# Performance work log

Measured on AMD Instinct MI355X. Metric: run time of the kernel, lower is better.

Reference implementation:

```python
import jax, jax.numpy as jnp
import numpy as np

# ---- config (mirrors init_kwargs) ----
H = 128
W = 128
FMO_STEPS = 4
INPUT_FRAMES = 1
N_PIECES = 1
N_TERMS = 2
CAM_DIST = 2.0
ROT_DIVIDE = 1.0
SIGMAINV = 7000.0
ERODE_K = 5
FOCAL = float(1.0 / np.tan(1.57 / 4.0))  # generate_perspective_projection(1.57/2), aspect=1


def quaternion_to_angle_axis(q):
    # q: [B,4] in (w,x,y,z) convention (torchgeometry)
    q1, q2, q3 = q[..., 1], q[..., 2], q[..., 3]
    sin_sq = q1 * q1 + q2 * q2 + q3 * q3
    sin_t = jnp.sqrt(sin_sq + 1e-20)
    cos_t = q[..., 0]
    two_theta = 2.0 * jnp.where(cos_t < 0.0, jnp.arctan2(-sin_t, -cos_t), jnp.arctan2(sin_t, cos_t))
    k = jnp.where(sin_sq > 1e-12, two_theta / sin_t, 2.0)
    return q[..., 1:4] * k[..., None]


def angle_axis_to_rotation_matrix(aa):
    # aa: [B,3] -> [B,3,3] (Rodrigues)
    th = jnp.sqrt(jnp.sum(aa * aa, axis=-1, keepdims=True) + 1e-12)  # [B,1]
    k = aa / th
    kx, ky, kz = k[..., 0], k[..., 1], k[..., 2]
    zero = jnp.zeros_like(kx)
    K = jnp.stack([jnp.stack([zero, -kz, ky], -1),
                   jnp.stack([kz, zero, -kx], -1),
                   jnp.stack([-ky, kx, zero], -1)], -2)
    s = jnp.sin(th)[..., None]
    c = jnp.cos(th)[..., None]
    return jnp.eye(3, dtype=aa.dtype) + s * K + (1.0 - c) * jnp.matmul(K, K)


def rasterize(fv_img, fv_z, face_feat, fn_z):
    # fv_img [B,F,3,2] NDC, fv_z [B,F,3] camera z, face_feat [B,F,3,C], fn_z [B,F]
    B, F = fv_img.shape[:2]
    xs = jnp.linspace(-1.0, 1.0, W)
    ys = jnp.linspace(1.0, -1.0, H)
    py, px = jnp.meshgrid(ys, xs, indexing='ij')  # [H,W]
    a, b, c = fv_img[:, :, 0], fv_img[:, :, 1], fv_img[:, :, 2]  # [B,F,2]
    e0 = b - a
    e1 = c - a
    denom = e0[..., 0] * e1[..., 1] - e0[..., 1] * e1[..., 0]  # [B,F]
    valid = (fn_z > 0.0) & (jnp.abs(denom) > 1e-10)
    inv_den = jnp.where(jnp.abs(denom) > 1e-10, 1.0 / denom, 0.0)
    dx = px[None, None] - a[..., 0][..., None, None]  # [B,F,H,W]
    dy = py[None, None] - a[..., 1][..., None, None]
    w1 = (dx * e1[..., 1][..., None, None] - dy * e1[..., 0][..., None, None]) * inv_den[..., None, None]
    w2 = (e0[..., 0][..., None, None] * dy - e0[..., 1][..., None, None] * dx) * inv_den[..., None, None]
    w0 = 1.0 - w1 - w2
    inside = (w0 >= 0.0) & (w1 >= 0.0) & (w2 >= 0.0) & valid[..., None, None]
    zi = (w0 * fv_z[:, :, 0, None, None] + w1 * fv_z[:, :, 1, None, None] + w2 * fv_z[:, :, 2, None, None])
    score = jnp.where(inside, zi, -1e10)  # camera looks down -z: nearest face has max z
    best = jnp.argmax(score, axis=1)      # [B,H,W] z-buffer winner
    hit = jnp.any(inside, axis=1)
    bary = jnp.stack([w0, w1, w2], axis=-1)  # [B,F,H,W,3]
    idx = jnp.broadcast_to(best[:, None, :, :, None], (B, 1, H, W, 3))
    bary_b = jnp.take_along_axis(bary, idx, axis=1)[:, 0]  # [B,H,W,3]
    feat_b = jax.vmap(lambda f, i: f[i])(face_feat, best)  # [B,H,W,3,C]
    feats = jnp.einsum('bhwkc,bhwk->bhwc', feat_b, bary_b) * hit[..., None]
    # DIB-R soft silhouette: A = 1 - prod(1 - exp(-sigmainv*d^2)), d = dist to triangle, 0 inside
    d2 = None
    tri = (a, b, c)
    for i in range(3):
        p, q = tri[i], tri[(i + 1) % 3]
        ex = (q - p)[..., 0][..., None, None]
        ey = (q - p)[..., 1][..., None, None]
        rx = px[None, None] - p[..., 0][..., None, None]
        ry = py[None, None] - p[..., 1][..., None, None]
        L2 = ex * ex + ey * ey + 1e-12
        t = jnp.clip((rx * ex + ry * ey) / L2, 0.0, 1.0)
        dxe = rx - t * ex
        dye = ry - t * ey
        dd = dxe * dxe + dye * dye
        d2 = dd if d2 is None else jnp.minimum(d2, dd)
    d2 = jnp.where(inside, 0.0, d2)
    prob = jnp.where(valid[..., None, None], jnp.exp(-SIGMAINV * d2), 0.0)
    mask = 1.0 - jnp.prod(1.0 - prob, axis=1)  # [B,H,W]
    return feats, mask


def texture_sample(tex, uv):
    # tex [B,3,Th,Tw], uv [B,H,W,2] in [0,1]; bilinear, v axis flipped (image row 0 <-> v=1)
    Th, Tw = tex.shape[2], tex.shape[3]
    u = jnp.clip(uv[..., 0], 0.0, 1.0) * (Tw - 1)
    v = (1.0 - jnp.clip(uv[..., 1], 0.0, 1.0)) * (Th - 1)
    x0 = jnp.floor(u)
    y0 = jnp.floor(v)
    fx = (u - x0)[:, None]  # [B,1,H,W]
    fy = (v - y0)[:, None]
    x0i = jnp.clip(x0.astype(jnp.int32), 0, Tw - 1)
    x1i = jnp.clip(x0i + 1, 0, Tw - 1)
    y0i = jnp.clip(y0.astype(jnp.int32), 0, Th - 1)
    y1i = jnp.clip(y0i + 1, 0, Th - 1)
    g = jax.vmap(lambda t, yy, xx: t[:, yy, xx])  # [B,3,H,W]
    t00 = g(tex, y0i, x0i)
    t01 = g(tex, y0i, x1i)
    t10 = g(tex, y1i, x0i)
    t11 = g(tex, y1i, x1i)
    return t00 * (1 - fx) * (1 - fy) + t01 * fx * (1 - fy) + t10 * (1 - fx) * fy + t11 * fx * fy


def erode(m, k):
    # kornia erosion with an all-ones kxk kernel == min-pool (geodesic border)
    return -jax.lax.reduce_window(-m, -jnp.inf, jax.lax.max, (1, k, k), (1, 1, 1), 'SAME')


def render_frame(verts_world, faces, face_features, texture_maps):
    # camera at (0,0,CAM_DIST) looking at origin with up=(0,1,0): R_cam == I
    v_cam = verts_world - jnp.array([0.0, 0.0, CAM_DIST], dtype=verts_world.dtype)
    fv_cam = v_cam[:, faces]  # [B,F,3,3]
    n = jnp.cross(fv_cam[:, :, 1] - fv_cam[:, :, 0], fv_cam[:, :, 2] - fv_cam[:, :, 0])
    n = n / (jnp.linalg.norm(n, axis=-1, keepdims=True) + 1e-10)
    fn_z = n[..., 2]
    z = fv_cam[..., 2]  # negative in front of camera
    img = FOCAL * fv_cam[..., :2] / (-z[..., None] + 1e-10)  # [B,F,3,2]
    uv, mask = rasterize(img, z, face_features, fn_z)
    rgb = texture_sample(texture_maps, uv)  # [B,3,H,W]
    mask_e = erode(mask, ERODE_K)
    return jnp.concatenate([rgb, mask_e[:, None]], axis=1)  # [B,4,H,W]


def reference(vertices, translation, quaternion, exp, face_features, texture_maps, faces):
    rot = angle_axis_to_rotation_matrix(quaternion_to_angle_axis(quaternion[:, 0, 0]))
    trans_start = translation[:, :, 0, 0]  # [B,1,3]
    all_renders = []
    renders = []
    frames = 0
    time_before = 0.0
    for pind in range(N_PIECES):
        angles = quaternion_to_angle_axis(quaternion[:, pind, 1]) / ROT_DIVIDE
        rot_step = angle_axis_to_rotation_matrix(exp * angles / FMO_STEPS)
        rot_noexp = angle_axis_to_rotation_matrix(angles * (1.0 - exp))
        n_steps = FMO_STEPS * INPUT_FRAMES // N_PIECES  # prop[pind] (forced for single piece)
        for ti in np.linspace(0.0, 1.0, n_steps):
            if frames == 0:
                time_before = ti
            time_exp = time_before + (ti - time_before) * exp  # [1]
            verts = jnp.einsum('bij,bvj->bvi', rot, vertices) + trans_start
            for p in range(1, N_TERMS):
                verts = verts + (time_exp ** p) * translation[:, :, pind, p]
            renders.append(render_frame(verts, faces, face_features, texture_maps))
            frames += 1
            if frames == FMO_STEPS:
                frames = 0
                all_renders.append(jnp.stack(renders, 1))
                renders = []
                rot = jnp.matmul(rot, rot_noexp)
            else:
                rot = jnp.matmul(rot, rot_step)
        for p in range(1, N_TERMS):
            trans_start = trans_start + translation[:, :, pind, p]
    return jnp.stack(all_renders, 1)  # [B, input_frames, fmo_steps, 4, H, W]


def setup_inputs() -> dict:
    key = jax.random.key(0)
    ks = jax.random.split(key, 7)
    B, V, F = 1, 162, 320
    vertices = jax.random.normal(ks[0], (B, V, 3), jnp.float32) * 0.3
    translation = jax.random.normal(ks[1], (B, 1, N_PIECES, N_TERMS, 3), jnp.float32) * 0.1
    quaternion = jax.random.normal(ks[2], (B, N_PIECES, 2, 4), jnp.float32)
    exp = jax.random.uniform(ks[3], (1,), jnp.float32)
    face_features = jax.random.uniform(ks[4], (B, F, 3, 2), jnp.float32)
    texture_maps = jax.random.uniform(ks[5], (B, 3, 256, 256), jnp.float32)
    faces = jax.random.randint(ks[6], (F, 3), 0, V)
    return {"vertices": vertices, "translation": translation, "quaternion": quaternion,
            "exp": exp, "face_features": face_features, "texture_maps": texture_maps,
            "faces": faces}
```

## Files before the change

### kernel.cpp

```cpp
#include <hip/hip_runtime.h>
#include <math.h>

#define N_FRAMES 4
#define N_FACES  320
#define N_VERTS  162
#define IMG_H    128
#define IMG_W    128
#define FD_STRIDE 24
#define NWAVES   8



__device__ __forceinline__ void q_to_aa(const float* q, float* aa) {
    float q1 = q[1], q2 = q[2], q3 = q[3];
    float sin_sq = (q1 * q1 + q2 * q2) + q3 * q3;
    float sin_t = sqrtf(sin_sq + 1e-20f);
    float cos_t = q[0];
    float two_theta = (cos_t < 0.0f) ? (2.0f * atan2f(-sin_t, -cos_t))
                                     : (2.0f * atan2f(sin_t, cos_t));
    float k = (sin_sq > 1e-12f) ? (two_theta / sin_t) : 2.0f;
    aa[0] = q1 * k; aa[1] = q2 * k; aa[2] = q3 * k;
}

__device__ __forceinline__ void aa_to_R(const float* aa, float* R) {
    float th = sqrtf(((aa[0] * aa[0] + aa[1] * aa[1]) + aa[2] * aa[2]) + 1e-12f);
    float kx = aa[0] / th, ky = aa[1] / th, kz = aa[2] / th;
    float K[9] = { 0.0f, -kz,  ky,
                   kz,  0.0f, -kx,
                  -ky,   kx, 0.0f };
    float s = sinf(th), c = cosf(th);
    float KK[9];
    for (int i = 0; i < 3; ++i)
        for (int j = 0; j < 3; ++j)
            KK[i*3+j] = (K[i*3+0] * K[0*3+j] + K[i*3+1] * K[1*3+j]) + K[i*3+2] * K[2*3+j];
    float omc = 1.0f - c;
    for (int i = 0; i < 9; ++i) {
        float eye = (i == 0 || i == 4 || i == 8) ? 1.0f : 0.0f;
        R[i] = (eye + s * K[i]) + omc * KK[i];
    }
}

__device__ __forceinline__ void mat3mul(const float* A, const float* B, float* C) {
    for (int i = 0; i < 3; ++i)
        for (int j = 0; j < 3; ++j)
            C[i*3+j] = (A[i*3+0] * B[0*3+j] + A[i*3+1] * B[1*3+j]) + A[i*3+2] * B[2*3+j];
}


__global__ void __launch_bounds__(256)
setup_kernel(const float* __restrict__ verts_in,
             const float* __restrict__ transl,
             const float* __restrict__ quat,
             const float* __restrict__ expv,
             const int*   __restrict__ faces,
             int*   __restrict__ faceCount,
             float* __restrict__ faceData)
{
    __shared__ float rots[N_FRAMES][9];
    __shared__ float sv[N_FRAMES][N_VERTS * 3];
    int tid = threadIdx.x;

    if (tid == 0) {
        float aa0[3], aa1[3], R0[9], step[9];
        q_to_aa(quat, aa0);
        aa_to_R(aa0, R0);
        q_to_aa(quat + 4, aa1);
        float e = expv[0];
        float arg[3];
        for (int i = 0; i < 3; ++i) arg[i] = (e * aa1[i]) / 4.0f;
        aa_to_R(arg, step);
        float cur[9];
        for (int i = 0; i < 9; ++i) { cur[i] = R0[i]; rots[0][i] = R0[i]; }
        for (int k = 1; k < N_FRAMES; ++k) {
            float nxt[9];
            mat3mul(cur, step, nxt);
            for (int i = 0; i < 9; ++i) { cur[i] = nxt[i]; rots[k][i] = nxt[i]; }
        }
    }
    __syncthreads();

    float e = expv[0];
    float t0 = transl[0], t1 = transl[1], t2 = transl[2];
    float u0 = transl[3], u1 = transl[4], u2 = transl[5];

    for (int item = tid; item < N_FRAMES * N_VERTS; item += blockDim.x) {
        int k = item / N_VERTS, v = item - k * N_VERTS;
        float te = (float)((double)k / 3.0) * e;
        float vx = verts_in[v*3+0], vy = verts_in[v*3+1], vz = verts_in[v*3+2];
        const float* R = rots[k];
        float dx_ = (R[0] * vx + R[1] * vy) + R[2] * vz;
        float dy_ = (R[3] * vx + R[4] * vy) + R[5] * vz;
        float dz_ = (R[6] * vx + R[7] * vy) + R[8] * vz;
        float x = (dx_ + t0) + te * u0;
        float y = (dy_ + t1) + te * u1;
        float z = (dz_ + t2) + te * u2;
        z = z - 2.0f;
        sv[k][v*3+0] = x; sv[k][v*3+1] = y; sv[k][v*3+2] = z;
    }
    __syncthreads();

    const float FOCAL = (float)(1.0 / tan(1.57 / 4.0));

    int w    = tid >> 6;
    int lane = tid & 63;
    unsigned long long lmask = (lane == 63) ? 0x7fffffffffffffffull
                                            : ((1ull << lane) - 1ull);
    int cnt = 0;
    for (int base = 0; base < N_FACES; base += 64) {
        int f = base + lane;
        int i0 = faces[f*3+0], i1 = faces[f*3+1], i2 = faces[f*3+2];
        const float* A = &sv[w][i0*3];
        const float* B = &sv[w][i1*3];
        const float* C = &sv[w][i2*3];
        float ux = B[0] - A[0], uy = B[1] - A[1];
        float wx = C[0] - A[0], wy = C[1] - A[1];
        float nz = ux * wy - uy * wx;
        float da = -A[2] + 1e-10f, db = -B[2] + 1e-10f, dc = -C[2] + 1e-10f;
        float ax = (FOCAL * A[0]) / da, ay = (FOCAL * A[1]) / da;
        float bx = (FOCAL * B[0]) / db, by = (FOCAL * B[1]) / db;
        float cx = (FOCAL * C[0]) / dc, cy = (FOCAL * C[1]) / dc;
        float e0x = bx - ax, e0y = by - ay;
        float e1x = cx - ax, e1y = cy - ay;
        float e12x = cx - bx, e12y = cy - by;
        float den = e0x * e1y - e0y * e1x;
        bool dok = fabsf(den) > 1e-10f;
        bool valid = dok && (nz > 0.0f);
        unsigned long long m = __ballot(valid);
        if (valid) {
            float invden = 1.0f / den;
            float L2_0 = (e0x * e0x + e0y * e0y) + 1e-12f;
            float L2_1 = (e12x * e12x + e12y * e12y) + 1e-12f;
            float L2_2 = (e1x * e1x + e1y * e1y) + 1e-12f;
            int pos = cnt + __popcll(m & lmask);
            float4* fd = (float4*)(faceData + (w * N_FACES + pos) * FD_STRIDE);
            fd[0] = make_float4(ax, ay, e0x, e0y);
            fd[1] = make_float4(e1x, e1y, invden, (float)f);
            fd[2] = make_float4(A[2], B[2], C[2], 1.0f / L2_0);
            fd[3] = make_float4(bx, by, e12x, e12y);
            fd[4] = make_float4(cx, cy, 1.0f / L2_1, 1.0f / L2_2);
            fd[5] = make_float4(fminf(fminf(ax, bx), cx), fminf(fminf(ay, by), cy),
                                fmaxf(fmaxf(ax, bx), cx), fmaxf(fmaxf(ay, by), cy));
        }
        cnt += __popcll(m);
    }
    if (lane == 0) faceCount[w] = cnt;
}


__global__ void __launch_bounds__(512)
raster_kernel(const int*   __restrict__ faceCount,
              const float* __restrict__ faceData,
              const float* __restrict__ ffeat,
              const float* __restrict__ tex,
              float* __restrict__ out,
              float* __restrict__ maskbuf)
{
    int frame = blockIdx.x >> 8;
    int blk   = blockIdx.x & 255;
    int tid   = threadIdx.x;
    int lane  = tid & 63;
    int wv    = __builtin_amdgcn_readfirstlane(tid >> 6);
    int tile_x = blk & 7, tile_y = blk >> 3;
    int j = tile_x * 16 + (lane & 15);
    int i = tile_y * 4 + (lane >> 4);

    int nv = faceCount[frame];

    float px = (float)(-1.0 + 2.0 * (double)j / 127.0);
    float py = (float)( 1.0 - 2.0 * (double)i / 127.0);

    float best = -1e10f;
    int bestf = 0;
    float bw0 = 0.0f, bw1 = 0.0f, bw2 = 0.0f;
    float P = 1.0f;

    const float* g = faceData + frame * N_FACES * FD_STRIDE;

    for (int f = wv; f < nv; f += NWAVES) {
        const float* d = g + f * FD_STRIDE;
        float xmin = d[20], ymin = d[21], xmax = d[22], ymax = d[23];
        float cdx = fmaxf(fmaxf(xmin - px, px - xmax), 0.0f);
        float cdy = fmaxf(fmaxf(ymin - py, py - ymax), 0.0f);
        bool near = (cdx * cdx + cdy * cdy) <= 0.003f;
        if (!__any(near)) continue;

        float ax = d[0], ay = d[1], e0x = d[2], e0y = d[3];
        float e1x = d[4], e1y = d[5], invden = d[6], fidx = d[7];
        float z0 = d[8], z1 = d[9], z2 = d[10], invL2_0 = d[11];
        float bx = d[12], by = d[13], e12x = d[14], e12y = d[15];
        float cx = d[16], cy = d[17], invL2_1 = d[18], invL2_2 = d[19];

        float dx = px - ax, dy = py - ay;
        float w1 = (dx * e1y - dy * e1x) * invden;
        float w2 = (e0x * dy - e0y * dx) * invden;
        float w0 = (1.0f - w1) - w2;
        bool inside = (w0 >= 0.0f) & (w1 >= 0.0f) & (w2 >= 0.0f);
        float zi = (w0 * z0 + w1 * z1) + w2 * z2;
        float score = inside ? zi : -1e10f;
        if (score > best) {
            best = score; bestf = (int)fidx; bw0 = w0; bw1 = w1; bw2 = w2;
        }

        float t0 = fminf(fmaxf((dx * e0x + dy * e0y) * invL2_0, 0.0f), 1.0f);
        float x0 = dx - t0 * e0x, y0 = dy - t0 * e0y;
        float dd = x0 * x0 + y0 * y0;
        float rx1 = px - bx, ry1 = py - by;
        float t1 = fminf(fmaxf((rx1 * e12x + ry1 * e12y) * invL2_1, 0.0f), 1.0f);
        float x1 = rx1 - t1 * e12x, y1 = ry1 - t1 * e12y;
        dd = fminf(dd, x1 * x1 + y1 * y1);
        float ex2 = -e1x, ey2 = -e1y;
        float rx2 = px - cx, ry2 = py - cy;
        float t2 = fminf(fmaxf((rx2 * ex2 + ry2 * ey2) * invL2_2, 0.0f), 1.0f);
        float x2 = rx2 - t2 * ex2, y2 = ry2 - t2 * ey2;
        dd = fminf(dd, x2 * x2 + y2 * y2);

        float d2 = inside ? 0.0f : dd;
        float prob = __expf(-7000.0f * d2);
        P *= (1.0f - prob);
    }

    __shared__ float red[512 * 6];
    float* my = &red[tid * 6];
    my[0] = best; my[1] = __int_as_float(bestf);
    my[2] = bw0;  my[3] = bw1; my[4] = bw2; my[5] = P;
    __syncthreads();

    if (tid < 64) {
        float bb = red[tid * 6 + 0];
        int   bf = __float_as_int(red[tid * 6 + 1]);
        float r0 = red[tid * 6 + 2], r1 = red[tid * 6 + 3], r2 = red[tid * 6 + 4];
        float Pt = red[tid * 6 + 5];
        for (int w = 1; w < NWAVES; ++w) {
            const float* e = &red[(w * 64 + tid) * 6];
            float s = e[0]; int ff = __float_as_int(e[1]);
            if ((s > bb) || ((s == bb) && (ff < bf))) {
                bb = s; bf = ff; r0 = e[2]; r1 = e[3]; r2 = e[4];
            }
            Pt *= e[5];
        }

        bool hit = bb != -1e10f;
        float uv0 = 0.0f, uv1 = 0.0f;
        if (hit) {
            const float* fp = ffeat + bf * 6;
            uv0 = (fp[0] * r0 + fp[2] * r1) + fp[4] * r2;
            uv1 = (fp[1] * r0 + fp[3] * r1) + fp[5] * r2;
        }
        float u = fminf(fmaxf(uv0, 0.0f), 1.0f) * 255.0f;
        float v = (1.0f - fminf(fmaxf(uv1, 0.0f), 1.0f)) * 255.0f;
        float x0f = floorf(u), y0f = floorf(v);
        float fx = u - x0f, fy = v - y0f;
        int x0i = min(max((int)x0f, 0), 255);
        int x1i = min(x0i + 1, 255);
        int y0i = min(max((int)y0f, 0), 255);
        int y1i = min(y0i + 1, 255);

        for (int c = 0; c < 3; ++c) {
            const float* tc = tex + c * 65536;
            float t00 = tc[y0i * 256 + x0i];
            float t01 = tc[y0i * 256 + x1i];
            float t10 = tc[y1i * 256 + x0i];
            float t11 = tc[y1i * 256 + x1i];
            float val = (t00 * (1.0f - fx)) * (1.0f - fy);
            val = val + (t01 * fx) * (1.0f - fy);
            val = val + (t10 * (1.0f - fx)) * fy;
            val = val + (t11 * fx) * fy;
            out[((frame * 4 + c) * IMG_H + i) * IMG_W + j] = val;
        }
        maskbuf[(frame * IMG_H + i) * IMG_W + j] = 1.0f - Pt;
    }
}


__global__ void __launch_bounds__(256)
erode_kernel(const float* __restrict__ maskbuf, float* __restrict__ out)
{
    int frame = blockIdx.x >> 6;
    int pix = (blockIdx.x & 63) * 256 + threadIdx.x;
    int i = pix >> 7, j = pix & 127;
    float m = 1e30f;
    for (int di = -2; di <= 2; ++di) {
        int ii = i + di;
        if (ii < 0 || ii >= IMG_H) continue;
        for (int dj = -2; dj <= 2; ++dj) {
            int jj = j + dj;
            if (jj < 0 || jj >= IMG_W) continue;
            m = fminf(m, maskbuf[(frame * IMG_H + ii) * IMG_W + jj]);
        }
    }
    out[((frame * 4 + 3) * IMG_H + i) * IMG_W + j] = m;
}


extern "C" void kernel_launch(void* const* d_in, const int* in_sizes, int n_in,
                              void* d_out, int out_size, void* d_ws, size_t ws_size,
                              hipStream_t stream) {
    const float* vertices      = (const float*)d_in[0];
    const float* translation   = (const float*)d_in[1];
    const float* quaternion    = (const float*)d_in[2];
    const float* expv          = (const float*)d_in[3];
    const float* face_features = (const float*)d_in[4];
    const float* texture_maps  = (const float*)d_in[5];
    const int*   faces         = (const int*)d_in[6];
    float* out = (float*)d_out;

    int*   faceCount = (int*)d_ws;
    float* faceData  = (float*)d_ws + 4;
    float* maskbuf   = faceData + N_FRAMES * N_FACES * FD_STRIDE;

    setup_kernel<<<1, 256, 0, stream>>>(vertices, translation, quaternion, expv,
                                        faces, faceCount, faceData);
    raster_kernel<<<N_FRAMES * 256, 512, 0, stream>>>(faceCount, faceData,
                                                      face_features, texture_maps,
                                                      out, maskbuf);
    erode_kernel<<<N_FRAMES * 64, 256, 0, stream>>>(maskbuf, out);
}
```

Measured before the change: 91.67 us.

## Fuse face setup into raster kernel with per-block LDS face records and tile culling

```diff
diff --git a/kernel.cpp b/kernel.cpp
--- a/kernel.cpp
+++ b/kernel.cpp
@@ -6,8 +6,15 @@
 #define N_VERTS  162
 #define IMG_H    128
 #define IMG_W    128
-#define FD_STRIDE 24
 #define NWAVES   8
+#define FPW      40
+#define REC_SZ   20
+
+#define SV_OFF   0
+#define BB_OFF   1952
+#define BB_LD    48
+#define REC_OFF  8096
+#define ARENA_SZ 33696
 
 
 
@@ -47,114 +54,23 @@
 }
 
 
-__global__ void __launch_bounds__(256)
-setup_kernel(const float* __restrict__ verts_in,
-             const float* __restrict__ transl,
-             const float* __restrict__ quat,
-             const float* __restrict__ expv,
-             const int*   __restrict__ faces,
-             int*   __restrict__ faceCount,
-             float* __restrict__ faceData)
-{
-    __shared__ float rots[N_FRAMES][9];
-    __shared__ float sv[N_FRAMES][N_VERTS * 3];
-    int tid = threadIdx.x;
-
-    if (tid == 0) {
-        float aa0[3], aa1[3], R0[9], step[9];
-        q_to_aa(quat, aa0);
-        aa_to_R(aa0, R0);
-        q_to_aa(quat + 4, aa1);
-        float e = expv[0];
-        float arg[3];
-        for (int i = 0; i < 3; ++i) arg[i] = (e * aa1[i]) / 4.0f;
-        aa_to_R(arg, step);
-        float cur[9];
-        for (int i = 0; i < 9; ++i) { cur[i] = R0[i]; rots[0][i] = R0[i]; }
-        for (int k = 1; k < N_FRAMES; ++k) {
-            float nxt[9];
-            mat3mul(cur, step, nxt);
-            for (int i = 0; i < 9; ++i) { cur[i] = nxt[i]; rots[k][i] = nxt[i]; }
-        }
-    }
-    __syncthreads();
-
-    float e = expv[0];
-    float t0 = transl[0], t1 = transl[1], t2 = transl[2];
-    float u0 = transl[3], u1 = transl[4], u2 = transl[5];
-
-    for (int item = tid; item < N_FRAMES * N_VERTS; item += blockDim.x) {
-        int k = item / N_VERTS, v = item - k * N_VERTS;
-        float te = (float)((double)k / 3.0) * e;
-        float vx = verts_in[v*3+0], vy = verts_in[v*3+1], vz = verts_in[v*3+2];
-        const float* R = rots[k];
-        float dx_ = (R[0] * vx + R[1] * vy) + R[2] * vz;
-        float dy_ = (R[3] * vx + R[4] * vy) + R[5] * vz;
-        float dz_ = (R[6] * vx + R[7] * vy) + R[8] * vz;
-        float x = (dx_ + t0) + te * u0;
-        float y = (dy_ + t1) + te * u1;
-        float z = (dz_ + t2) + te * u2;
-        z = z - 2.0f;
-        sv[k][v*3+0] = x; sv[k][v*3+1] = y; sv[k][v*3+2] = z;
-    }
-    __syncthreads();
-
-    const float FOCAL = (float)(1.0 / tan(1.57 / 4.0));
-
-    int w    = tid >> 6;
-    int lane = tid & 63;
-    unsigned long long lmask = (lane == 63) ? 0x7fffffffffffffffull
-                                            : ((1ull << lane) - 1ull);
-    int cnt = 0;
-    for (int base = 0; base < N_FACES; base += 64) {
-        int f = base + lane;
-        int i0 = faces[f*3+0], i1 = faces[f*3+1], i2 = faces[f*3+2];
-        const float* A = &sv[w][i0*3];
-        const float* B = &sv[w][i1*3];
-        const float* C = &sv[w][i2*3];
-        float ux = B[0] - A[0], uy = B[1] - A[1];
-        float wx = C[0] - A[0], wy = C[1] - A[1];
-        float nz = ux * wy - uy * wx;
-        float da = -A[2] + 1e-10f, db = -B[2] + 1e-10f, dc = -C[2] + 1e-10f;
-        float ax = (FOCAL * A[0]) / da, ay = (FOCAL * A[1]) / da;
-        float bx = (FOCAL * B[0]) / db, by = (FOCAL * B[1]) / db;
-        float cx = (FOCAL * C[0]) / dc, cy = (FOCAL * C[1]) / dc;
-        float e0x = bx - ax, e0y = by - ay;
-        float e1x = cx - ax, e1y = cy - ay;
-        float e12x = cx - bx, e12y = cy - by;
-        float den = e0x * e1y - e0y * e1x;
-        bool dok = fabsf(den) > 1e-10f;
-        bool valid = dok && (nz > 0.0f);
-        unsigned long long m = __ballot(valid);
-        if (valid) {
-            float invden = 1.0f / den;
-            float L2_0 = (e0x * e0x + e0y * e0y) + 1e-12f;
-            float L2_1 = (e12x * e12x + e12y * e12y) + 1e-12f;
-            float L2_2 = (e1x * e1x + e1y * e1y) + 1e-12f;
-            int pos = cnt + __popcll(m & lmask);
-            float4* fd = (float4*)(faceData + (w * N_FACES + pos) * FD_STRIDE);
-            fd[0] = make_float4(ax, ay, e0x, e0y);
-            fd[1] = make_float4(e1x, e1y, invden, (float)f);
-            fd[2] = make_float4(A[2], B[2], C[2], 1.0f / L2_0);
-            fd[3] = make_float4(bx, by, e12x, e12y);
-            fd[4] = make_float4(cx, cy, 1.0f / L2_1, 1.0f / L2_2);
-            fd[5] = make_float4(fminf(fminf(ax, bx), cx), fminf(fminf(ay, by), cy),
-                                fmaxf(fmaxf(ax, bx), cx), fmaxf(fmaxf(ay, by), cy));
-        }
-        cnt += __popcll(m);
-    }
-    if (lane == 0) faceCount[w] = cnt;
-}
-
-
 __global__ void __launch_bounds__(512)
-raster_kernel(const int*   __restrict__ faceCount,
-              const float* __restrict__ faceData,
+render_kernel(const float* __restrict__ verts_in,
+              const float* __restrict__ transl,
+              const float* __restrict__ quat,
+              const float* __restrict__ expv,
+              const int*   __restrict__ faces,
               const float* __restrict__ ffeat,
               const float* __restrict__ tex,
               float* __restrict__ out,
               float* __restrict__ maskbuf)
 {
+    __shared__ __align__(16) char arena[ARENA_SZ];
+    float* sv   = (float*)(arena + SV_OFF);
+    float* bb   = (float*)(arena + BB_OFF);
+    float* recs = (float*)(arena + REC_OFF);
+    float* red  = (float*)arena;
+
     int frame = blockIdx.x >> 8;
     int blk   = blockIdx.x & 255;
     int tid   = threadIdx.x;
@@ -164,25 +80,115 @@
     int j = tile_x * 16 + (lane & 15);
     int i = tile_y * 4 + (lane >> 4);
 
-    int nv = faceCount[frame];
+    float e = expv[0];
+    float R[9];
+    {
+        float aa0[3], aa1[3], S[9];
+        q_to_aa(quat, aa0);
+        aa_to_R(aa0, R);
+        q_to_aa(quat + 4, aa1);
+        float arg[3];
+        for (int t = 0; t < 3; ++t) arg[t] = (e * aa1[t]) / 4.0f;
+        aa_to_R(arg, S);
+        for (int t = 0; t < frame; ++t) {
+            float nxt[9];
+            mat3mul(R, S, nxt);
+            for (int q = 0; q < 9; ++q) R[q] = nxt[q];
+        }
+    }
+
+    if (tid < N_VERTS) {
+        float te = (float)((double)frame / 3.0) * e;
+        float vx = verts_in[tid*3+0], vy = verts_in[tid*3+1], vz = verts_in[tid*3+2];
+        float dx_ = (R[0] * vx + R[1] * vy) + R[2] * vz;
+        float dy_ = (R[3] * vx + R[4] * vy) + R[5] * vz;
+        float dz_ = (R[6] * vx + R[7] * vy) + R[8] * vz;
+        float x = (dx_ + transl[0]) + te * transl[3];
+        float y = (dy_ + transl[1]) + te * transl[4];
+        float z = (dz_ + transl[2]) + te * transl[5];
+        z = z - 2.0f;
+        sv[tid*3+0] = x; sv[tid*3+1] = y; sv[tid*3+2] = z;
+    }
+    __syncthreads();
+
+    const float FOCAL = (float)(1.0 / tan(1.57 / 4.0));
+    int cnt;
+    {
+        bool valid = false;
+        float ax=0, ay=0, bx=0, by=0, cx=0, cy=0, e0x=0, e0y=0, e1x=0, e1y=0;
+        float e12x=0, e12y=0, z0=0, z1=0, z2=0, den=0;
+        int f = wv * FPW + lane;
+        if (lane < FPW) {
+            int i0 = faces[f*3+0], i1 = faces[f*3+1], i2 = faces[f*3+2];
+            const float* A = &sv[i0*3];
+            const float* B = &sv[i1*3];
+            const float* C = &sv[i2*3];
+            float ux = B[0] - A[0], uy = B[1] - A[1];
+            float wx = C[0] - A[0], wy = C[1] - A[1];
+            float nz = ux * wy - uy * wx;
+            float da = -A[2] + 1e-10f, db = -B[2] + 1e-10f, dc = -C[2] + 1e-10f;
+            ax = (FOCAL * A[0]) / da; ay = (FOCAL * A[1]) / da;
+            bx = (FOCAL * B[0]) / db; by = (FOCAL * B[1]) / db;
+            cx = (FOCAL * C[0]) / dc; cy = (FOCAL * C[1]) / dc;
+            e0x = bx - ax; e0y = by - ay;
+            e1x = cx - ax; e1y = cy - ay;
+            e12x = cx - bx; e12y = cy - by;
+            den = e0x * e1y - e0y * e1x;
+            z0 = A[2]; z1 = B[2]; z2 = C[2];
+            valid = (fabsf(den) > 1e-10f) && (nz > 0.0f);
+        }
+        unsigned long long m = __ballot(valid);
+        cnt = __popcll(m);
+        if (valid) {
+            unsigned long long lmask = (lane == 63) ? 0x7fffffffffffffffull
+                                                    : ((1ull << lane) - 1ull);
+            int pos = __popcll(m & lmask);
+            float invden = 1.0f / den;
+            float L2_0 = (e0x * e0x + e0y * e0y) + 1e-12f;
+            float L2_1 = (e12x * e12x + e12y * e12y) + 1e-12f;
+            float L2_2 = (e1x * e1x + e1y * e1y) + 1e-12f;
+            float4* r = (float4*)&recs[(wv * FPW + pos) * REC_SZ];
+            r[0] = make_float4(ax, ay, e0x, e0y);
+            r[1] = make_float4(e1x, e1y, invden, (float)f);
+            r[2] = make_float4(z0, z1, z2, 1.0f / L2_0);
+            r[3] = make_float4(bx, by, e12x, e12y);
+            r[4] = make_float4(cx, cy, 1.0f / L2_1, 1.0f / L2_2);
+            float* wbb = &bb[wv * 4 * BB_LD];
+            wbb[0*BB_LD + pos] = fminf(fminf(ax, bx), cx);
+            wbb[1*BB_LD + pos] = fminf(fminf(ay, by), cy);
+            wbb[2*BB_LD + pos] = fmaxf(fmaxf(ax, bx), cx);
+            wbb[3*BB_LD + pos] = fmaxf(fmaxf(ay, by), cy);
+        }
+    }
 
     float px = (float)(-1.0 + 2.0 * (double)j / 127.0);
     float py = (float)( 1.0 - 2.0 * (double)i / 127.0);
+    float txmin = (float)(-1.0 + 2.0 * (double)(tile_x * 16) / 127.0);
+    float txmax = (float)(-1.0 + 2.0 * (double)(tile_x * 16 + 15) / 127.0);
+    float tymax = (float)( 1.0 - 2.0 * (double)(tile_y * 4) / 127.0);
+    float tymin = (float)( 1.0 - 2.0 * (double)(tile_y * 4 + 3) / 127.0);
+
+    unsigned long long fmask;
+    {
+        int l = (lane < FPW) ? lane : 0;
+        const float* wbb = &bb[wv * 4 * BB_LD];
+        float xmin = wbb[0*BB_LD + l], ymin = wbb[1*BB_LD + l];
+        float xmax = wbb[2*BB_LD + l], ymax = wbb[3*BB_LD + l];
+        float cdx = fmaxf(fmaxf(xmin - txmax, txmin - xmax), 0.0f);
+        float cdy = fmaxf(fmaxf(ymin - tymax, tymin - ymax), 0.0f);
+        bool near = ((cdx * cdx + cdy * cdy) <= 0.0026f) && (lane < cnt);
+        fmask = __ballot(near);
+    }
 
     float best = -1e10f;
     int bestf = 0;
     float bw0 = 0.0f, bw1 = 0.0f, bw2 = 0.0f;
     float P = 1.0f;
 
-    const float* g = faceData + frame * N_FACES * FD_STRIDE;
-
-    for (int f = wv; f < nv; f += NWAVES) {
-        const float* d = g + f * FD_STRIDE;
-        float xmin = d[20], ymin = d[21], xmax = d[22], ymax = d[23];
-        float cdx = fmaxf(fmaxf(xmin - px, px - xmax), 0.0f);
-        float cdy = fmaxf(fmaxf(ymin - py, py - ymax), 0.0f);
-        bool near = (cdx * cdx + cdy * cdy) <= 0.003f;
-        if (!__any(near)) continue;
+    while (fmask) {
+        int fc = __ffsll((unsigned long long)fmask) - 1;
+        fmask &= fmask - 1;
+        const float* d = &recs[(wv * FPW + fc) * REC_SZ];
 
         float ax = d[0], ay = d[1], e0x = d[2], e0y = d[3];
         float e1x = d[4], e1y = d[5], invden = d[6], fidx = d[7];
@@ -219,27 +225,27 @@
         P *= (1.0f - prob);
     }
 
-    __shared__ float red[512 * 6];
+    __syncthreads();
     float* my = &red[tid * 6];
     my[0] = best; my[1] = __int_as_float(bestf);
     my[2] = bw0;  my[3] = bw1; my[4] = bw2; my[5] = P;
     __syncthreads();
 
     if (tid < 64) {
-        float bb = red[tid * 6 + 0];
-        int   bf = __float_as_int(red[tid * 6 + 1]);
+        float bbst = red[tid * 6 + 0];
+        int   bf   = __float_as_int(red[tid * 6 + 1]);
         float r0 = red[tid * 6 + 2], r1 = red[tid * 6 + 3], r2 = red[tid * 6 + 4];
         float Pt = red[tid * 6 + 5];
         for (int w = 1; w < NWAVES; ++w) {
-            const float* e = &red[(w * 64 + tid) * 6];
-            float s = e[0]; int ff = __float_as_int(e[1]);
-            if ((s > bb) || ((s == bb) && (ff < bf))) {
-                bb = s; bf = ff; r0 = e[2]; r1 = e[3]; r2 = e[4];
+            const float* s = &red[(w * 64 + tid) * 6];
+            float sc = s[0]; int ff = __float_as_int(s[1]);
+            if ((sc > bbst) || ((sc == bbst) && (ff < bf))) {
+                bbst = sc; bf = ff; r0 = s[2]; r1 = s[3]; r2 = s[4];
             }
-            Pt *= e[5];
-        }
-
-        bool hit = bb != -1e10f;
+            Pt *= s[5];
+        }
+
+        bool hit = bbst != -1e10f;
         float uv0 = 0.0f, uv1 = 0.0f;
         if (hit) {
             const float* fp = ffeat + bf * 6;
@@ -304,13 +310,10 @@
     const int*   faces         = (const int*)d_in[6];
     float* out = (float*)d_out;
 
-    int*   faceCount = (int*)d_ws;
-    float* faceData  = (float*)d_ws + 4;
-    float* maskbuf   = faceData + N_FRAMES * N_FACES * FD_STRIDE;
-
-    setup_kernel<<<1, 256, 0, stream>>>(vertices, translation, quaternion, expv,
-                                        faces, faceCount, faceData);
-    raster_kernel<<<N_FRAMES * 256, 512, 0, stream>>>(faceCount, faceData,
+    float* maskbuf = (float*)d_ws;
+
+    render_kernel<<<N_FRAMES * 256, 512, 0, stream>>>(vertices, translation,
+                                                      quaternion, expv, faces,
                                                       face_features, texture_maps,
                                                       out, maskbuf);
     erode_kernel<<<N_FRAMES * 64, 256, 0, stream>>>(maskbuf, out);
```

New measurement: 90.15 us. No clear change (-1.7%).

## Bin faces per 8x8 tile via ballot masks and stage records in LDS

Applied to the files above, without the earlier changes.

```diff
diff --git a/kernel.cpp b/kernel.cpp
--- a/kernel.cpp
+++ b/kernel.cpp
@@ -6,8 +6,8 @@
 #define N_VERTS  162
 #define IMG_H    128
 #define IMG_W    128
-#define FD_STRIDE 24
-#define NWAVES   8
+#define REC_SZ   20
+#define NWAVES   4
 
 
 
@@ -54,7 +54,8 @@
              const float* __restrict__ expv,
              const int*   __restrict__ faces,
              int*   __restrict__ faceCount,
-             float* __restrict__ faceData)
+             float* __restrict__ bbg,
+             float* __restrict__ recsg)
 {
     __shared__ float rots[N_FRAMES][9];
     __shared__ float sv[N_FRAMES][N_VERTS * 3];
@@ -132,14 +133,16 @@
             float L2_1 = (e12x * e12x + e12y * e12y) + 1e-12f;
             float L2_2 = (e1x * e1x + e1y * e1y) + 1e-12f;
             int pos = cnt + __popcll(m & lmask);
-            float4* fd = (float4*)(faceData + (w * N_FACES + pos) * FD_STRIDE);
-            fd[0] = make_float4(ax, ay, e0x, e0y);
-            fd[1] = make_float4(e1x, e1y, invden, (float)f);
-            fd[2] = make_float4(A[2], B[2], C[2], 1.0f / L2_0);
-            fd[3] = make_float4(bx, by, e12x, e12y);
-            fd[4] = make_float4(cx, cy, 1.0f / L2_1, 1.0f / L2_2);
-            fd[5] = make_float4(fminf(fminf(ax, bx), cx), fminf(fminf(ay, by), cy),
-                                fmaxf(fmaxf(ax, bx), cx), fmaxf(fmaxf(ay, by), cy));
+            float4* r = (float4*)&recsg[(w * N_FACES + pos) * REC_SZ];
+            r[0] = make_float4(ax, ay, e0x, e0y);
+            r[1] = make_float4(e1x, e1y, invden, (float)f);
+            r[2] = make_float4(A[2], B[2], C[2], 1.0f / L2_0);
+            r[3] = make_float4(bx, by, e12x, e12y);
+            r[4] = make_float4(cx, cy, 1.0f / L2_1, 1.0f / L2_2);
+            bbg[(w * 4 + 0) * N_FACES + pos] = fminf(fminf(ax, bx), cx);
+            bbg[(w * 4 + 1) * N_FACES + pos] = fminf(fminf(ay, by), cy);
+            bbg[(w * 4 + 2) * N_FACES + pos] = fmaxf(fmaxf(ax, bx), cx);
+            bbg[(w * 4 + 3) * N_FACES + pos] = fmaxf(fmaxf(ay, by), cy);
         }
         cnt += __popcll(m);
     }
@@ -147,96 +150,129 @@
 }
 
 
-__global__ void __launch_bounds__(512)
+__global__ void __launch_bounds__(256)
 raster_kernel(const int*   __restrict__ faceCount,
-              const float* __restrict__ faceData,
+              const float* __restrict__ bbg,
+              const float* __restrict__ recsg,
               const float* __restrict__ ffeat,
               const float* __restrict__ tex,
               float* __restrict__ out,
               float* __restrict__ maskbuf)
 {
+    __shared__ float4 srecs[N_FACES * 5];
+    __shared__ float  sred[256 * 7];
+
     int frame = blockIdx.x >> 8;
-    int blk   = blockIdx.x & 255;
+    int t     = blockIdx.x & 255;
     int tid   = threadIdx.x;
     int lane  = tid & 63;
     int wv    = __builtin_amdgcn_readfirstlane(tid >> 6);
-    int tile_x = blk & 7, tile_y = blk >> 3;
-    int j = tile_x * 16 + (lane & 15);
-    int i = tile_y * 4 + (lane >> 4);
+    int tx = t & 15, ty = t >> 4;
+    int j = tx * 8 + (lane & 7);
+    int i = ty * 8 + (lane >> 3);
 
     int nv = faceCount[frame];
+    int rounds = (nv + 63) >> 6;
+
+    {
+        const float4* g = (const float4*)(recsg + frame * N_FACES * REC_SZ);
+        for (int idx = tid; idx < nv * 5; idx += 256) srecs[idx] = g[idx];
+    }
+    __syncthreads();
 
     float px = (float)(-1.0 + 2.0 * (double)j / 127.0);
     float py = (float)( 1.0 - 2.0 * (double)i / 127.0);
+
+    float txmin = (float)(-1.0 + 2.0 * (double)(tx * 8) / 127.0);
+    float txmax = (float)(-1.0 + 2.0 * (double)(tx * 8 + 7) / 127.0);
+    float tymax = (float)( 1.0 - 2.0 * (double)(ty * 8) / 127.0);
+    float tymin = (float)( 1.0 - 2.0 * (double)(ty * 8 + 7) / 127.0);
+
+    unsigned long long masks[5];
+    for (int c = 0; c < rounds; ++c) {
+        int f = c * 64 + lane;
+        bool near = false;
+        if (f < nv) {
+            float xmin = bbg[(frame * 4 + 0) * N_FACES + f];
+            float ymin = bbg[(frame * 4 + 1) * N_FACES + f];
+            float xmax = bbg[(frame * 4 + 2) * N_FACES + f];
+            float ymax = bbg[(frame * 4 + 3) * N_FACES + f];
+            float cdx = fmaxf(fmaxf(xmin - txmax, txmin - xmax), 0.0f);
+            float cdy = fmaxf(fmaxf(ymin - tymax, tymin - ymax), 0.0f);
+            near = (cdx * cdx + cdy * cdy) <= 0.0026f;
+        }
+        masks[c] = __ballot(near);
+    }
 
     float best = -1e10f;
     int bestf = 0;
     float bw0 = 0.0f, bw1 = 0.0f, bw2 = 0.0f;
     float P = 1.0f;
-
-    const float* g = faceData + frame * N_FACES * FD_STRIDE;
-
-    for (int f = wv; f < nv; f += NWAVES) {
-        const float* d = g + f * FD_STRIDE;
-        float xmin = d[20], ymin = d[21], xmax = d[22], ymax = d[23];
-        float cdx = fmaxf(fmaxf(xmin - px, px - xmax), 0.0f);
-        float cdy = fmaxf(fmaxf(ymin - py, py - ymax), 0.0f);
-        bool near = (cdx * cdx + cdy * cdy) <= 0.003f;
-        if (!__any(near)) continue;
-
-        float ax = d[0], ay = d[1], e0x = d[2], e0y = d[3];
-        float e1x = d[4], e1y = d[5], invden = d[6], fidx = d[7];
-        float z0 = d[8], z1 = d[9], z2 = d[10], invL2_0 = d[11];
-        float bx = d[12], by = d[13], e12x = d[14], e12y = d[15];
-        float cx = d[16], cy = d[17], invL2_1 = d[18], invL2_2 = d[19];
-
-        float dx = px - ax, dy = py - ay;
-        float w1 = (dx * e1y - dy * e1x) * invden;
-        float w2 = (e0x * dy - e0y * dx) * invden;
-        float w0 = (1.0f - w1) - w2;
-        bool inside = (w0 >= 0.0f) & (w1 >= 0.0f) & (w2 >= 0.0f);
-        float zi = (w0 * z0 + w1 * z1) + w2 * z2;
-        float score = inside ? zi : -1e10f;
-        if (score > best) {
-            best = score; bestf = (int)fidx; bw0 = w0; bw1 = w1; bw2 = w2;
-        }
-
-        float t0 = fminf(fmaxf((dx * e0x + dy * e0y) * invL2_0, 0.0f), 1.0f);
-        float x0 = dx - t0 * e0x, y0 = dy - t0 * e0y;
-        float dd = x0 * x0 + y0 * y0;
-        float rx1 = px - bx, ry1 = py - by;
-        float t1 = fminf(fmaxf((rx1 * e12x + ry1 * e12y) * invL2_1, 0.0f), 1.0f);
-        float x1 = rx1 - t1 * e12x, y1 = ry1 - t1 * e12y;
-        dd = fminf(dd, x1 * x1 + y1 * y1);
-        float ex2 = -e1x, ey2 = -e1y;
-        float rx2 = px - cx, ry2 = py - cy;
-        float t2 = fminf(fmaxf((rx2 * ex2 + ry2 * ey2) * invL2_2, 0.0f), 1.0f);
-        float x2 = rx2 - t2 * ex2, y2 = ry2 - t2 * ey2;
-        dd = fminf(dd, x2 * x2 + y2 * y2);
-
-        float d2 = inside ? 0.0f : dd;
-        float prob = __expf(-7000.0f * d2);
-        P *= (1.0f - prob);
-    }
-
-    __shared__ float red[512 * 6];
-    float* my = &red[tid * 6];
-    my[0] = best; my[1] = __int_as_float(bestf);
-    my[2] = bw0;  my[3] = bw1; my[4] = bw2; my[5] = P;
+    int sel = 0;
+
+    for (int c = 0; c < rounds; ++c) {
+        unsigned long long m = masks[c];
+        while (m) {
+            int b = __ffsll(m) - 1;
+            m &= m - 1;
+            if (((sel++) & 3) != wv) continue;
+            const float* d = (const float*)&srecs[(c * 64 + b) * 5];
+
+            float ax = d[0], ay = d[1], e0x = d[2], e0y = d[3];
+            float e1x = d[4], e1y = d[5], invden = d[6], fidx = d[7];
+            float z0 = d[8], z1 = d[9], z2 = d[10], invL2_0 = d[11];
+            float bx = d[12], by = d[13], e12x = d[14], e12y = d[15];
+            float cx = d[16], cy = d[17], invL2_1 = d[18], invL2_2 = d[19];
+
+            float dx = px - ax, dy = py - ay;
+            float w1 = (dx * e1y - dy * e1x) * invden;
+            float w2 = (e0x * dy - e0y * dx) * invden;
+            float w0 = (1.0f - w1) - w2;
+            bool inside = (w0 >= 0.0f) & (w1 >= 0.0f) & (w2 >= 0.0f);
+            float zi = (w0 * z0 + w1 * z1) + w2 * z2;
+            float score = inside ? zi : -1e10f;
+            if (score > best) {
+                best = score; bestf = (int)fidx; bw0 = w0; bw1 = w1; bw2 = w2;
+            }
+
+            float t0 = fminf(fmaxf((dx * e0x + dy * e0y) * invL2_0, 0.0f), 1.0f);
+            float x0 = dx - t0 * e0x, y0 = dy - t0 * e0y;
+            float dd = x0 * x0 + y0 * y0;
+            float rx1 = px - bx, ry1 = py - by;
+            float t1 = fminf(fmaxf((rx1 * e12x + ry1 * e12y) * invL2_1, 0.0f), 1.0f);
+            float x1 = rx1 - t1 * e12x, y1 = ry1 - t1 * e12y;
+            dd = fminf(dd, x1 * x1 + y1 * y1);
+            float ex2 = -e1x, ey2 = -e1y;
+            float rx2 = px - cx, ry2 = py - cy;
+            float t2 = fminf(fmaxf((rx2 * ex2 + ry2 * ey2) * invL2_2, 0.0f), 1.0f);
+            float x2 = rx2 - t2 * ex2, y2 = ry2 - t2 * ey2;
+            dd = fminf(dd, x2 * x2 + y2 * y2);
+
+            float d2 = inside ? 0.0f : dd;
+            float prob = __expf(-7000.0f * d2);
+            P *= (1.0f - prob);
+        }
+    }
+
+    {
+        float* my = &sred[tid * 7];
+        my[0] = best; my[1] = __int_as_float(bestf);
+        my[2] = bw0;  my[3] = bw1; my[4] = bw2; my[5] = P;
+    }
     __syncthreads();
 
     if (tid < 64) {
-        float bb = red[tid * 6 + 0];
-        int   bf = __float_as_int(red[tid * 6 + 1]);
-        float r0 = red[tid * 6 + 2], r1 = red[tid * 6 + 3], r2 = red[tid * 6 + 4];
-        float Pt = red[tid * 6 + 5];
+        float bb = sred[tid * 7 + 0];
+        int   bf = __float_as_int(sred[tid * 7 + 1]);
+        float r0 = sred[tid * 7 + 2], r1 = sred[tid * 7 + 3], r2 = sred[tid * 7 + 4];
+        float Pt = sred[tid * 7 + 5];
         for (int w = 1; w < NWAVES; ++w) {
-            const float* e = &red[(w * 64 + tid) * 6];
-            float s = e[0]; int ff = __float_as_int(e[1]);
-            if ((s > bb) || ((s == bb) && (ff < bf))) {
-                bb = s; bf = ff; r0 = e[2]; r1 = e[3]; r2 = e[4];
+            const float* s = &sred[(w * 64 + tid) * 7];
+            float sc = s[0]; int ff = __float_as_int(s[1]);
+            if ((sc > bb) || ((sc == bb) && (ff < bf))) {
+                bb = sc; bf = ff; r0 = s[2]; r1 = s[3]; r2 = s[4];
             }
-            Pt *= e[5];
+            Pt *= s[5];
         }
 
         bool hit = bb != -1e10f;
@@ -305,12 +341,13 @@
     float* out = (float*)d_out;
 
     int*   faceCount = (int*)d_ws;
-    float* faceData  = (float*)d_ws + 4;
-    float* maskbuf   = faceData + N_FRAMES * N_FACES * FD_STRIDE;
+    float* bbg       = (float*)d_ws + 4;
+    float* recsg     = bbg + 4 * 4 * N_FACES;
+    float* maskbuf   = recsg + 4 * N_FACES * REC_SZ;
 
     setup_kernel<<<1, 256, 0, stream>>>(vertices, translation, quaternion, expv,
-                                        faces, faceCount, faceData);
-    raster_kernel<<<N_FRAMES * 256, 512, 0, stream>>>(faceCount, faceData,
+                                        faces, faceCount, bbg, recsg);
+    raster_kernel<<<N_FRAMES * 256, 256, 0, stream>>>(faceCount, bbg, recsg,
                                                       face_features, texture_maps,
                                                       out, maskbuf);
     erode_kernel<<<N_FRAMES * 64, 256, 0, stream>>>(maskbuf, out);
```

Result: slower. 93.53 us (+2.0%).
